# Optimization experiments

Measured on AMD Instinct MI355X. Metric: run time of the kernel, lower is better.

## Reference

```python
import jax, jax.numpy as jnp
import numpy as np

N_EMBD = 768
N_HEAD = 12
N_LAYERS = 12
VOCAB = 50257
HEAD_DIM = N_EMBD // N_HEAD
D_FF = 4 * N_EMBD
B, S = 2, 1024


def setup_inputs() -> dict:
    key = jax.random.key(0)
    ks = jax.random.split(key, 8)
    w = lambda k, shape: jax.random.normal(k, shape, jnp.float32) * 0.02
    return {
        "x": jax.random.normal(ks[0], (B, S, N_EMBD), jnp.float32),
        "Wqkv": w(ks[1], (N_LAYERS, N_EMBD, 3 * N_EMBD)),
        "bqkv": jnp.zeros((N_LAYERS, 3 * N_EMBD), jnp.float32),
        "Wo": w(ks[2], (N_LAYERS, N_EMBD, N_EMBD)),
        "bo": jnp.zeros((N_LAYERS, N_EMBD), jnp.float32),
        "W1": w(ks[3], (N_LAYERS, N_EMBD, D_FF)),
        "b1": jnp.zeros((N_LAYERS, D_FF), jnp.float32),
        "W2": w(ks[4], (N_LAYERS, D_FF, N_EMBD)),
        "b2": jnp.zeros((N_LAYERS, N_EMBD), jnp.float32),
        "ln1_g": jnp.ones((N_LAYERS, N_EMBD), jnp.float32),
        "ln1_b": jnp.zeros((N_LAYERS, N_EMBD), jnp.float32),
        "ln2_g": jnp.ones((N_LAYERS, N_EMBD), jnp.float32),
        "ln2_b": jnp.zeros((N_LAYERS, N_EMBD), jnp.float32),
        "lnf_g": jnp.ones((N_EMBD,), jnp.float32),
        "lnf_b": jnp.zeros((N_EMBD,), jnp.float32),
        "Wlm": w(ks[5], (VOCAB, N_EMBD)),
    }


def layer_norm(x, g, b, eps=1e-5):
    m = jnp.mean(x, axis=-1, keepdims=True)
    v = jnp.var(x, axis=-1, keepdims=True)
    return (x - m) * jax.lax.rsqrt(v + eps) * g + b


def reference(x, Wqkv, bqkv, Wo, bo, W1, b1, W2, b2,
              ln1_g, ln1_b, ln2_g, ln2_b, lnf_g, lnf_b, Wlm):
    b_, s_, d_ = x.shape
    # additive causal mask: (1 - tril) * -1e10
    mask = (1.0 - jnp.tril(jnp.ones((s_, s_), jnp.float32))) * -1e10
    scale = 1.0 / np.sqrt(HEAD_DIM).astype(np.float32)

    def block(h, p):
        wqkv, bq, wo, bo_, w1, b1_, w2, b2_, g1, be1, g2, be2 = p
        a = layer_norm(h, g1, be1)
        qkv = a @ wqkv + bq                      # [B,S,3D]
        q, k, v = jnp.split(qkv, 3, axis=-1)
        split = lambda t: t.reshape(b_, s_, N_HEAD, HEAD_DIM).transpose(0, 2, 1, 3)
        q, k, v = split(q), split(k), split(v)   # [B,H,S,hd]
        scores = jnp.einsum('bhqd,bhkd->bhqk', q, k) * scale + mask
        probs = jax.nn.softmax(scores, axis=-1)
        o = jnp.einsum('bhqk,bhkd->bhqd', probs, v)
        o = o.transpose(0, 2, 1, 3).reshape(b_, s_, d_)
        h = h + (o @ wo + bo_)                   # residual 1
        m = layer_norm(h, g2, be2)
        m = jax.nn.gelu(m @ w1 + b1_, approximate=False)  # torch nn.GELU (erf)
        h = h + (m @ w2 + b2_)                   # residual 2
        return h, None

    h, _ = jax.lax.scan(
        block, x,
        (Wqkv, bqkv, Wo, bo, W1, b1, W2, b2, ln1_g, ln1_b, ln2_g, ln2_b))
    h = layer_norm(h, lnf_g, lnf_b)
    return h @ Wlm.T                             # [B,S,VOCAB]
```

## Files before the change

kernel.cpp:

```cpp
#include <hip/hip_runtime.h>
#include <math.h>

typedef unsigned short u16;
typedef u16 u16x8 __attribute__((ext_vector_type(8)));
typedef u16 u16x4 __attribute__((ext_vector_type(4)));
typedef short short8 __attribute__((ext_vector_type(8)));
typedef float f32x4 __attribute__((ext_vector_type(4)));

#define NE 768
#define NH 12
#define NL 12
#define NV 50257
#define NVP 50432
#define HD 64
#define DFF 3072
#define NB 2
#define SL 1024
#define TT 2048
#define QKVD 2304

static __device__ __forceinline__ u16 f2bf(float f){
  unsigned int x; __builtin_memcpy(&x, &f, 4);
  x = (x + 0x7FFFu + ((x >> 16) & 1u)) >> 16;
  return (u16)x;
}

typedef const __attribute__((address_space(1))) unsigned int* gas1_t;
typedef __attribute__((address_space(3))) unsigned int* las3_t;
static __device__ __forceinline__ void gload16(const u16* g, u16* l){
  __builtin_amdgcn_global_load_lds((gas1_t)(const void*)g, (las3_t)(void*)l, 16, 0, 0);
}
static __device__ __forceinline__ void waitvm(int n){
  switch (n){
    case 0: asm volatile("s_waitcnt vmcnt(0)" ::: "memory"); break;
    case 3: asm volatile("s_waitcnt vmcnt(3)" ::: "memory"); break;
    case 4: asm volatile("s_waitcnt vmcnt(4)" ::: "memory"); break;
    case 6: asm volatile("s_waitcnt vmcnt(6)" ::: "memory"); break;
    default: asm volatile("s_waitcnt vmcnt(8)" ::: "memory"); break;
  }
}

__global__ void k_cvt4(const float4* __restrict__ in, u16x4* __restrict__ out, long n4){
  long i = (long)blockIdx.x * blockDim.x + threadIdx.x;
  long st = (long)gridDim.x * blockDim.x;
  for (; i < n4; i += st){
    float4 v = in[i];
    u16x4 o = { f2bf(v.x), f2bf(v.y), f2bf(v.z), f2bf(v.w) };
    out[i] = o;
  }
}

__global__ __launch_bounds__(256) void k_transpose_cvt_all(const float* __restrict__ in0,
    u16* __restrict__ out0, int K, int N){
  __shared__ u16 tile[32][33];
  const float* in = in0 + (long)blockIdx.z * K * N;
  u16* out = out0 + (long)blockIdx.z * N * K;
  int n0 = blockIdx.x * 32, k0 = blockIdx.y * 32;
#pragma unroll
  for (int i = 0; i < 4; ++i){
    int e = threadIdx.x + i * 256;
    int r = e >> 5, c = e & 31;
    tile[r][c] = f2bf(in[(long)(k0 + r) * N + (n0 + c)]);
  }
  __syncthreads();
#pragma unroll
  for (int i = 0; i < 4; ++i){
    int e = threadIdx.x + i * 256;
    int r = e >> 5, c = e & 31;
    out[(long)(n0 + r) * K + (k0 + c)] = tile[c][r];
  }
}

__global__ __launch_bounds__(256) void k_layernorm(const float* __restrict__ x,
    const float* __restrict__ g, const float* __restrict__ b, u16* __restrict__ out){
  int row = blockIdx.x;
  const float* xr = x + (long)row * NE;
  int t = threadIdx.x;
  float v[3];
  v[0] = xr[t]; v[1] = xr[t + 256]; v[2] = xr[t + 512];
  float s = v[0] + v[1] + v[2];
  float sq = v[0]*v[0] + v[1]*v[1] + v[2]*v[2];
  __shared__ float red[8];
#pragma unroll
  for (int o = 32; o; o >>= 1){ s += __shfl_xor(s, o); sq += __shfl_xor(sq, o); }
  int wid = t >> 6, lane = t & 63;
  if (!lane){ red[wid] = s; red[4 + wid] = sq; }
  __syncthreads();
  s  = red[0] + red[1] + red[2] + red[3];
  sq = red[4] + red[5] + red[6] + red[7];
  float mean = s * (1.f / NE);
  float var  = sq * (1.f / NE) - mean * mean;
  float rs = rsqrtf(var + 1e-5f);
  u16* orow = out + (long)row * NE;
#pragma unroll
  for (int i = 0; i < 3; ++i){
    int c = t + i * 256;
    orow[c] = f2bf((v[i] - mean) * rs * g[c] + b[c]);
  }
}

__global__ __launch_bounds__(256) void k_combine_ln(float* __restrict__ h,
    const float* __restrict__ part, const float* __restrict__ bias, int nsplit,
    const float* __restrict__ g, const float* __restrict__ b, u16* __restrict__ aout){
  int row = blockIdx.x;
  int t = threadIdx.x;
  float* hr = h + (long)row * NE;
  float v[3];
#pragma unroll
  for (int i = 0; i < 3; ++i){
    int c = t + i * 256;
    float acc = hr[c] + bias[c];
    for (int s = 0; s < nsplit; ++s)
      acc += part[(long)s * TT * NE + (long)row * NE + c];
    v[i] = acc;
    hr[c] = acc;
  }
  float s = v[0] + v[1] + v[2];
  float sq = v[0]*v[0] + v[1]*v[1] + v[2]*v[2];
  __shared__ float red[8];
#pragma unroll
  for (int o = 32; o; o >>= 1){ s += __shfl_xor(s, o); sq += __shfl_xor(sq, o); }
  int wid = t >> 6, lane = t & 63;
  if (!lane){ red[wid] = s; red[4 + wid] = sq; }
  __syncthreads();
  s  = red[0] + red[1] + red[2] + red[3];
  sq = red[4] + red[5] + red[6] + red[7];
  float mean = s * (1.f / NE);
  float var  = sq * (1.f / NE) - mean * mean;
  float rs = rsqrtf(var + 1e-5f);
  u16* orow = aout + (long)row * NE;
#pragma unroll
  for (int i = 0; i < 3; ++i){
    int c = t + i * 256;
    orow[c] = f2bf((v[i] - mean) * rs * g[c] + b[c]);
  }
}

__global__ __launch_bounds__(256) void k_flash(const u16* __restrict__ qkv,
    const u16* __restrict__ vt, u16* __restrict__ out){
  __shared__ u16 Ps[4][16][72];
  const int z = blockIdx.x;
  const int qt = gridDim.y - 1 - blockIdx.y;
  const int b = z / NH, h = z % NH;
  const int q0 = qt * 64;
  const int t = threadIdx.x, lane = t & 63, wid = t >> 6;
  const int lr = lane & 15, lk = lane >> 4;
  const int qr0 = q0 + wid * 16;
  const u16* Qp = qkv + (long)(b * SL + qr0 + lr) * QKVD + h * HD;
  short8 aq[2];
  aq[0] = *(const short8*)(Qp + lk * 8);
  aq[1] = *(const short8*)(Qp + 32 + lk * 8);
  const u16* Kb  = qkv + (long)(b * SL) * QKVD + NE + h * HD;
  const u16* Vtb = vt + (long)z * HD * SL;
  f32x4 o[4] = {};
  float m[4], l[4];
#pragma unroll
  for (int r = 0; r < 4; ++r){ m[r] = -3e38f; l[r] = 0.f; }
  const int nt = qt + 1;
  for (int kt = 0; kt < nt; ++kt){
    const int kv0 = kt * 64;
    short8 kb[4][2];
#pragma unroll
    for (int j = 0; j < 4; ++j)
#pragma unroll
      for (int c = 0; c < 2; ++c)
        kb[j][c] = *(const short8*)(Kb + (long)(kv0 + j * 16 + lr) * QKVD + c * 32 + lk * 8);
    f32x4 s[4] = {};
#pragma unroll
    for (int c = 0; c < 2; ++c)
#pragma unroll
      for (int j = 0; j < 4; ++j)
        s[j] = __builtin_amdgcn_mfma_f32_16x16x32_bf16(aq[c], kb[j][c], s[j], 0, 0, 0);
    const bool dm = (kt == nt - 1);
#pragma unroll
    for (int r = 0; r < 4; ++r){
      const int row = qr0 + lk * 4 + r;
      float pm = -3e38f;
#pragma unroll
      for (int j = 0; j < 4; ++j){
        float v = s[j][r] * 0.125f;
        if (dm && (kv0 + j * 16 + lr > row)) v = -3e38f;
        s[j][r] = v;
        pm = fmaxf(pm, v);
      }
#pragma unroll
      for (int off = 1; off < 16; off <<= 1) pm = fmaxf(pm, __shfl_xor(pm, off));
      float mn = fmaxf(m[r], pm);
      float f = __expf(m[r] - mn);
      m[r] = mn;
      float ps = 0.f;
#pragma unroll
      for (int j = 0; j < 4; ++j){
        float pv = __expf(s[j][r] - mn);
        ps += pv;
        Ps[wid][lk * 4 + r][j * 16 + lr] = f2bf(pv);
      }
#pragma unroll
      for (int off = 1; off < 16; off <<= 1) ps += __shfl_xor(ps, off);
      l[r] = l[r] * f + ps;
#pragma unroll
      for (int j = 0; j < 4; ++j) o[j][r] *= f;
    }
#pragma unroll
    for (int c = 0; c < 2; ++c){
      short8 pa = *(const short8*)&Ps[wid][lr][c * 32 + lk * 8];
#pragma unroll
      for (int j = 0; j < 4; ++j){
        short8 vb = *(const short8*)(Vtb + (long)(j * 16 + lr) * SL + kv0 + c * 32 + lk * 8);
        o[j] = __builtin_amdgcn_mfma_f32_16x16x32_bf16(pa, vb, o[j], 0, 0, 0);
      }
    }
  }
  u16* O = out + (long)(b * SL) * NE + h * HD;
#pragma unroll
  for (int r = 0; r < 4; ++r){
    float inv = 1.f / l[r];
    const int row = qr0 + lk * 4 + r;
#pragma unroll
    for (int j = 0; j < 4; ++j)
      O[(long)row * NE + j * 16 + lr] = f2bf(o[j][r] * inv);
  }
}

struct GemmP {
  const u16* A; const u16* B; void* C;
  const float* bias; u16* vt;
  int M, N, K, lda, ldb, ldc, mode;
  long zA, zB, zC;
};

__global__ __launch_bounds__(256) void k_gemm_bt(GemmP p){
  __shared__ u16 As[3][64 * 32];
  __shared__ u16 Bs[3][128 * 32];
  const int nwg = gridDim.x * gridDim.y;
  const int orig = blockIdx.x + blockIdx.y * gridDim.x;
  const int wg = (orig & 7) * (nwg >> 3) + (orig >> 3);
  const int m0 = (wg % gridDim.x) * 64, n0 = (wg / gridDim.x) * 128;
  const u16* A = p.A + (long)blockIdx.z * p.zA;
  const u16* B = p.B + (long)blockIdx.z * p.zB;
  const long offC = (long)blockIdx.z * p.zC;
  const int t = threadIdx.x, lane = t & 63, wid = t >> 6;
  const int wm = (wid >> 1) * 32, wn = (wid & 1) * 64;
  const int lr = lane & 15, lk = lane >> 4;
  const int srow = t >> 2;
  const int sseg = (t & 3) * 8;
  const u16* Abase  = A + (long)(m0 + srow) * p.lda + sseg;
  const u16* Bbase  = B + (long)(n0 + srow) * p.ldb + sseg;
  const u16* Bbase2 = B + (long)(n0 + 64 + srow) * p.ldb + sseg;
  auto stage = [&](int buf, int kt){
    gload16(Abase  + kt * 32, &As[buf][t * 8]);
    gload16(Bbase  + kt * 32, &Bs[buf][t * 8]);
    gload16(Bbase2 + kt * 32, &Bs[buf][(t + 256) * 8]);
  };
  f32x4 acc[2][4] = {};
  const int nk = p.K >> 5;
  stage(0, 0);
  stage(1, 1);
  int cur = 0;
  for (int kt = 0; kt < nk; ++kt){
    if (kt + 2 < nk){
      int nxt = cur + 2; if (nxt >= 3) nxt -= 3;
      stage(nxt, kt + 2);
    }
    int rem = nk - 1 - kt;
    waitvm(rem >= 2 ? 6 : rem == 1 ? 3 : 0);
    __builtin_amdgcn_s_barrier();
    short8 af[2], bfr[4];
#pragma unroll
    for (int i = 0; i < 2; ++i) af[i]  = *(const short8*)&As[cur][(wm + i * 16 + lr) * 32 + lk * 8];
#pragma unroll
    for (int j = 0; j < 4; ++j) bfr[j] = *(const short8*)&Bs[cur][(wn + j * 16 + lr) * 32 + lk * 8];
#pragma unroll
    for (int i = 0; i < 2; ++i)
#pragma unroll
      for (int j = 0; j < 4; ++j)
        acc[i][j] = __builtin_amdgcn_mfma_f32_16x16x32_bf16(af[i], bfr[j], acc[i][j], 0, 0, 0);
    asm volatile("s_waitcnt lgkmcnt(0)" ::: "memory");
    __builtin_amdgcn_s_barrier();
    cur = (cur == 2) ? 0 : cur + 1;
  }
#pragma unroll
  for (int i = 0; i < 2; ++i){
#pragma unroll
    for (int r = 0; r < 4; ++r){
      int row = m0 + wm + i * 16 + lk * 4 + r;
      if (row >= p.M) continue;
#pragma unroll
      for (int j = 0; j < 4; ++j){
        int col = n0 + wn + j * 16 + lr;
        if (col >= p.N) continue;
        float v = acc[i][j][r];
        long idx = offC + (long)row * p.ldc + col;
        if (p.mode == 5){
          v += p.bias[col];
          if (col >= 2 * NE){
            int d = col - 2 * NE;
            long vidx = (((long)(row >> 10) * NH + (d >> 6)) * HD + (d & 63)) * SL + (row & 1023);
            p.vt[vidx] = f2bf(v);
          } else {
            ((u16*)p.C)[idx] = f2bf(v);
          }
        } else if (p.mode == 2){
          v += p.bias[col];
          v = 0.5f * v * (1.f + erff(v * 0.70710678118f));
          ((u16*)p.C)[idx] = f2bf(v);
        } else {
          ((float*)p.C)[idx] = v;
        }
      }
    }
  }
}

static inline void gemm(hipStream_t s, const u16* A, int lda, const u16* B, int ldb,
    void* C, int ldc, int M, int N, int K, const float* bias, u16* vt, int mode,
    int gz = 1, long zA = 0, long zB = 0, long zC = 0){
  GemmP p{ A, B, C, bias, vt, M, N, K, lda, ldb, ldc, mode, zA, zB, zC };
  dim3 g(M / 64, (N + 127) / 128, gz);
  k_gemm_bt<<<g, 256, 0, s>>>(p);
}

__global__ __launch_bounds__(1024, 4) void k_gemm256(const u16* __restrict__ A,
    const u16* __restrict__ B, float* __restrict__ C){
  __shared__ u16 As[2][256 * 64];
  __shared__ u16 Bs[2][256 * 64];
  const int gx = gridDim.x, nwg = gx * gridDim.y;
  const int orig = blockIdx.x + blockIdx.y * gx;
  const int wg = (orig & 7) * (nwg >> 3) + (orig >> 3);
  const int m0 = (wg % gx) * 256, n0 = (wg / gx) * 256;
  const int t = threadIdx.x, lane = t & 63;
  const int lr = lane & 15, lk = lane >> 4;
  const int wid = t >> 6, wr = wid >> 2, wc = wid & 3;
  const u16* gA[2]; const u16* gB[2]; int ldst[2];
#pragma unroll
  for (int i = 0; i < 2; ++i){
    int tt = t + i * 1024, r = tt >> 3, pp = tt & 7, sl = pp ^ (r & 7);
    gA[i] = A + (long)(m0 + r) * NE + sl * 8;
    gB[i] = B + (long)(n0 + r) * NE + sl * 8;
    ldst[i] = tt * 8;
  }
  auto stage = [&](int buf, int kt){
#pragma unroll
    for (int i = 0; i < 2; ++i) gload16(gA[i] + kt * 64, &As[buf][ldst[i]]);
#pragma unroll
    for (int i = 0; i < 2; ++i) gload16(gB[i] + kt * 64, &Bs[buf][ldst[i]]);
  };
  f32x4 acc[4][4] = {};
  const int nk = NE / 64;
  stage(0, 0);
  for (int kt = 0; kt < nk; ++kt){
    const int buf = kt & 1;
    if (kt + 1 < nk){ stage(buf ^ 1, kt + 1); waitvm(4); }
    else            { waitvm(0); }
    __builtin_amdgcn_sched_barrier(0);
    __builtin_amdgcn_s_barrier();
    __builtin_amdgcn_sched_barrier(0);
    short8 bf[4][2];
#pragma unroll
    for (int nj = 0; nj < 4; ++nj)
#pragma unroll
      for (int kc = 0; kc < 2; ++kc){
        int r = wc * 64 + nj * 16 + lr;
        bf[nj][kc] = *(const short8*)&Bs[buf][r * 64 + ((kc * 32 + lk * 8) ^ ((r & 7) << 3))];
      }
#pragma unroll
    for (int mh = 0; mh < 2; ++mh){
      short8 af[2][2];
#pragma unroll
      for (int mi = 0; mi < 2; ++mi)
#pragma unroll
        for (int kc = 0; kc < 2; ++kc){
          int r = wr * 64 + (mh * 2 + mi) * 16 + lr;
          af[mi][kc] = *(const short8*)&As[buf][r * 64 + ((kc * 32 + lk * 8) ^ ((r & 7) << 3))];
        }
      __builtin_amdgcn_s_setprio(1);
#pragma unroll
      for (int mi = 0; mi < 2; ++mi)
#pragma unroll
        for (int nj = 0; nj < 4; ++nj)
#pragma unroll
          for (int kc = 0; kc < 2; ++kc)
            acc[mh * 2 + mi][nj] = __builtin_amdgcn_mfma_f32_16x16x32_bf16(af[mi][kc], bf[nj][kc], acc[mh * 2 + mi][nj], 0, 0, 0);
      __builtin_amdgcn_s_setprio(0);
    }
    asm volatile("s_waitcnt lgkmcnt(0)" ::: "memory");
    __builtin_amdgcn_sched_barrier(0);
    __builtin_amdgcn_s_barrier();
  }
#pragma unroll
  for (int mi = 0; mi < 4; ++mi)
#pragma unroll
    for (int r = 0; r < 4; ++r){
      int row = m0 + wr * 64 + mi * 16 + lk * 4 + r;
#pragma unroll
      for (int nj = 0; nj < 4; ++nj){
        int col = n0 + wc * 64 + nj * 16 + lr;
        if (col < NV) C[(long)row * NV + col] = acc[mi][nj][r];
      }
    }
}

extern "C" void kernel_launch(void* const* d_in, const int* in_sizes, int n_in,
                              void* d_out, int out_size, void* d_ws, size_t ws_size,
                              hipStream_t stream){
  (void)in_sizes; (void)n_in; (void)out_size; (void)ws_size;
  const float* x    = (const float*)d_in[0];
  const float* Wqkv = (const float*)d_in[1];
  const float* bqkv = (const float*)d_in[2];
  const float* Wo   = (const float*)d_in[3];
  const float* bo   = (const float*)d_in[4];
  const float* W1   = (const float*)d_in[5];
  const float* b1   = (const float*)d_in[6];
  const float* W2   = (const float*)d_in[7];
  const float* b2   = (const float*)d_in[8];
  const float* ln1g = (const float*)d_in[9];
  const float* ln1b = (const float*)d_in[10];
  const float* ln2g = (const float*)d_in[11];
  const float* ln2b = (const float*)d_in[12];
  const float* lnfg = (const float*)d_in[13];
  const float* lnfb = (const float*)d_in[14];
  const float* Wlm  = (const float*)d_in[15];

  char* ws = (char*)d_ws;
  size_t off = 0;
  auto alloc = [&](size_t bytes){ void* p = ws + off; off += (bytes + 255) & ~255UL; return p; };
  float* h      = (float*)alloc((size_t)TT * NE * 4);
  u16*   a      = (u16*)  alloc((size_t)TT * NE * 2);
  u16*   qkv    = (u16*)  alloc((size_t)TT * QKVD * 2);
  u16*   vtbuf  = (u16*)  alloc((size_t)NB * NH * HD * SL * 2);
  u16*   attno  = (u16*)  alloc((size_t)TT * NE * 2);
  u16*   ffm    = (u16*)  alloc((size_t)TT * DFF * 2);
  float* part   = (float*)alloc((size_t)4 * TT * NE * 4);
  u16*   wqkvT  = (u16*)  alloc((size_t)NL * QKVD * NE * 2);
  u16*   woT    = (u16*)  alloc((size_t)NL * NE * NE * 2);
  u16*   w1T    = (u16*)  alloc((size_t)NL * DFF * NE * 2);
  u16*   w2T    = (u16*)  alloc((size_t)NL * NE * DFF * 2);
  u16*   wlmB   = (u16*)  alloc((size_t)NVP * NE * 2);

  hipMemcpyAsync(h, x, (size_t)TT * NE * 4, hipMemcpyDeviceToDevice, stream);
  k_transpose_cvt_all<<<dim3(QKVD / 32, NE / 32, NL), 256, 0, stream>>>(Wqkv, wqkvT, NE, QKVD);
  k_transpose_cvt_all<<<dim3(NE / 32, NE / 32, NL),   256, 0, stream>>>(Wo,   woT,   NE, NE);
  k_transpose_cvt_all<<<dim3(DFF / 32, NE / 32, NL),  256, 0, stream>>>(W1,   w1T,   NE, DFF);
  k_transpose_cvt_all<<<dim3(NE / 32, DFF / 32, NL),  256, 0, stream>>>(W2,   w2T,   DFF, NE);
  k_cvt4<<<2048, 256, 0, stream>>>((const float4*)Wlm, (u16x4*)wlmB, (long)NV * NE / 4);
  hipMemsetAsync(wlmB + (size_t)NV * NE, 0, (size_t)(NVP - NV) * NE * 2, stream);

  k_layernorm<<<TT, 256, 0, stream>>>(h, ln1g, ln1b, a);

  for (int L = 0; L < NL; ++L){
    gemm(stream, a, NE, wqkvT + (size_t)L * QKVD * NE, NE, qkv, QKVD, TT, QKVD, NE,
         bqkv + (size_t)L * QKVD, vtbuf, 5);
    k_flash<<<dim3(NB * NH, SL / 64), 256, 0, stream>>>(qkv, vtbuf, attno);
    gemm(stream, attno, NE, woT + (size_t)L * NE * NE, NE, part, NE, TT, NE, 384,
         nullptr, nullptr, 3, 2, 384, 384, (long)TT * NE);
    k_combine_ln<<<TT, 256, 0, stream>>>(h, part, bo + (size_t)L * NE, 2,
         ln2g + (size_t)L * NE, ln2b + (size_t)L * NE, a);
    gemm(stream, a, NE, w1T + (size_t)L * DFF * NE, NE, ffm, DFF, TT, DFF, NE,
         b1 + (size_t)L * DFF, nullptr, 2);
    gemm(stream, ffm, DFF, w2T + (size_t)L * NE * DFF, DFF, part, NE, TT, NE, 768,
         nullptr, nullptr, 3, 4, 768, 768, (long)TT * NE);
    const float* gn = (L + 1 < NL) ? ln1g + (size_t)(L + 1) * NE : lnfg;
    const float* bn = (L + 1 < NL) ? ln1b + (size_t)(L + 1) * NE : lnfb;
    k_combine_ln<<<TT, 256, 0, stream>>>(h, part, b2 + (size_t)L * NE, 4, gn, bn, a);
  }
  k_gemm256<<<dim3(TT / 256, NVP / 256), 1024, 0, stream>>>(a, wlmB, (float*)d_out);
}
```

Baseline: 2.509 ms.

## Halve flash query tile and retile LM-head GEMM with triple-buffered K=32 stages

The flash-attention kernel now uses 32-row query tiles with two waves per block instead of 64 rows with four. This doubles the grid and cuts wasted causal work in the last KV tile. The LM-head GEMM moves from 1024 threads with a K=64 double buffer to 512 threads, each wave covering 128x64 outputs, with a K=32 triple-buffered pipeline and a 4-way swizzle. This trades more accumulator registers per thread and lower occupancy for deeper prefetch and more MFMA work per LDS fragment.

Result: no change. 2.474 ms (-1.4%).

```diff
diff --git a/kernel.cpp b/kernel.cpp
--- a/kernel.cpp
+++ b/kernel.cpp
@@ -136,16 +136,15 @@
   }
 }
 
-__global__ __launch_bounds__(256) void k_flash(const u16* __restrict__ qkv,
+__global__ __launch_bounds__(128) void k_flash(const u16* __restrict__ qkv,
     const u16* __restrict__ vt, u16* __restrict__ out){
-  __shared__ u16 Ps[4][16][72];
+  __shared__ u16 Ps[2][16][72];
   const int z = blockIdx.x;
   const int qt = gridDim.y - 1 - blockIdx.y;
   const int b = z / NH, h = z % NH;
-  const int q0 = qt * 64;
   const int t = threadIdx.x, lane = t & 63, wid = t >> 6;
   const int lr = lane & 15, lk = lane >> 4;
-  const int qr0 = q0 + wid * 16;
+  const int qr0 = qt * 32 + wid * 16;
   const u16* Qp = qkv + (long)(b * SL + qr0 + lr) * QKVD + h * HD;
   short8 aq[2];
   aq[0] = *(const short8*)(Qp + lk * 8);
@@ -156,7 +155,7 @@
   float m[4], l[4];
 #pragma unroll
   for (int r = 0; r < 4; ++r){ m[r] = -3e38f; l[r] = 0.f; }
-  const int nt = qt + 1;
+  const int nt = (qt * 32 + 31) / 64 + 1;
   for (int kt = 0; kt < nt; ++kt){
     const int kv0 = kt * 64;
     short8 kb[4][2];
@@ -320,10 +319,10 @@
   k_gemm_bt<<<g, 256, 0, s>>>(p);
 }
 
-__global__ __launch_bounds__(1024, 4) void k_gemm256(const u16* __restrict__ A,
+__global__ __launch_bounds__(512, 1) void k_gemm256(const u16* __restrict__ A,
     const u16* __restrict__ B, float* __restrict__ C){
-  __shared__ u16 As[2][256 * 64];
-  __shared__ u16 Bs[2][256 * 64];
+  __shared__ u16 As[3][256 * 32];
+  __shared__ u16 Bs[3][256 * 32];
   const int gx = gridDim.x, nwg = gx * gridDim.y;
   const int orig = blockIdx.x + blockIdx.y * gx;
   const int wg = (orig & 7) * (nwg >> 3) + (orig >> 3);
@@ -334,64 +333,78 @@
   const u16* gA[2]; const u16* gB[2]; int ldst[2];
 #pragma unroll
   for (int i = 0; i < 2; ++i){
-    int tt = t + i * 1024, r = tt >> 3, pp = tt & 7, sl = pp ^ (r & 7);
+    int idx = t + i * 512, r = idx >> 2, pp = idx & 3, sl = pp ^ (r & 3);
     gA[i] = A + (long)(m0 + r) * NE + sl * 8;
     gB[i] = B + (long)(n0 + r) * NE + sl * 8;
-    ldst[i] = tt * 8;
+    ldst[i] = idx * 8;
   }
   auto stage = [&](int buf, int kt){
 #pragma unroll
-    for (int i = 0; i < 2; ++i) gload16(gA[i] + kt * 64, &As[buf][ldst[i]]);
-#pragma unroll
-    for (int i = 0; i < 2; ++i) gload16(gB[i] + kt * 64, &Bs[buf][ldst[i]]);
+    for (int i = 0; i < 2; ++i) gload16(gA[i] + kt * 32, &As[buf][ldst[i]]);
+#pragma unroll
+    for (int i = 0; i < 2; ++i) gload16(gB[i] + kt * 32, &Bs[buf][ldst[i]]);
   };
-  f32x4 acc[4][4] = {};
-  const int nk = NE / 64;
+  f32x4 acc[8][4] = {};
+  const int nk = NE / 32;
   stage(0, 0);
+  stage(1, 1);
+  int cur = 0;
   for (int kt = 0; kt < nk; ++kt){
-    const int buf = kt & 1;
-    if (kt + 1 < nk){ stage(buf ^ 1, kt + 1); waitvm(4); }
-    else            { waitvm(0); }
+    if (kt + 2 < nk){
+      int nxt = cur + 2; if (nxt >= 3) nxt -= 3;
+      stage(nxt, kt + 2);
+    }
+    int rem = nk - 1 - kt;
+    waitvm(rem >= 2 ? 8 : rem == 1 ? 4 : 0);
     __builtin_amdgcn_sched_barrier(0);
     __builtin_amdgcn_s_barrier();
     __builtin_amdgcn_sched_barrier(0);
-    short8 bf[4][2];
-#pragma unroll
-    for (int nj = 0; nj < 4; ++nj)
-#pragma unroll
-      for (int kc = 0; kc < 2; ++kc){
-        int r = wc * 64 + nj * 16 + lr;
-        bf[nj][kc] = *(const short8*)&Bs[buf][r * 64 + ((kc * 32 + lk * 8) ^ ((r & 7) << 3))];
-      }
-#pragma unroll
-    for (int mh = 0; mh < 2; ++mh){
-      short8 af[2][2];
-#pragma unroll
-      for (int mi = 0; mi < 2; ++mi)
-#pragma unroll
-        for (int kc = 0; kc < 2; ++kc){
-          int r = wr * 64 + (mh * 2 + mi) * 16 + lr;
-          af[mi][kc] = *(const short8*)&As[buf][r * 64 + ((kc * 32 + lk * 8) ^ ((r & 7) << 3))];
-        }
+    short8 bf[4];
+#pragma unroll
+    for (int nj = 0; nj < 4; ++nj){
+      int r = wc * 64 + nj * 16 + lr;
+      bf[nj] = *(const short8*)&Bs[cur][r * 32 + ((lk ^ (r & 3)) * 8)];
+    }
+    {
+      short8 af[4];
+#pragma unroll
+      for (int mi = 0; mi < 4; ++mi){
+        int r = wr * 128 + mi * 16 + lr;
+        af[mi] = *(const short8*)&As[cur][r * 32 + ((lk ^ (r & 3)) * 8)];
+      }
       __builtin_amdgcn_s_setprio(1);
 #pragma unroll
-      for (int mi = 0; mi < 2; ++mi)
+      for (int mi = 0; mi < 4; ++mi)
 #pragma unroll
         for (int nj = 0; nj < 4; ++nj)
-#pragma unroll
-          for (int kc = 0; kc < 2; ++kc)
-            acc[mh * 2 + mi][nj] = __builtin_amdgcn_mfma_f32_16x16x32_bf16(af[mi][kc], bf[nj][kc], acc[mh * 2 + mi][nj], 0, 0, 0);
+          acc[mi][nj] = __builtin_amdgcn_mfma_f32_16x16x32_bf16(af[mi], bf[nj], acc[mi][nj], 0, 0, 0);
+      __builtin_amdgcn_s_setprio(0);
+    }
+    {
+      short8 af[4];
+#pragma unroll
+      for (int mi = 0; mi < 4; ++mi){
+        int r = wr * 128 + (mi + 4) * 16 + lr;
+        af[mi] = *(const short8*)&As[cur][r * 32 + ((lk ^ (r & 3)) * 8)];
+      }
+      __builtin_amdgcn_s_setprio(1);
+#pragma unroll
+      for (int mi = 0; mi < 4; ++mi)
+#pragma unroll
+        for (int nj = 0; nj < 4; ++nj)
+          acc[mi + 4][nj] = __builtin_amdgcn_mfma_f32_16x16x32_bf16(af[mi], bf[nj], acc[mi + 4][nj], 0, 0, 0);
       __builtin_amdgcn_s_setprio(0);
     }
     asm volatile("s_waitcnt lgkmcnt(0)" ::: "memory");
     __builtin_amdgcn_sched_barrier(0);
     __builtin_amdgcn_s_barrier();
-  }
-#pragma unroll
-  for (int mi = 0; mi < 4; ++mi)
+    cur = (cur == 2) ? 0 : cur + 1;
+  }
+#pragma unroll
+  for (int mi = 0; mi < 8; ++mi)
 #pragma unroll
     for (int r = 0; r < 4; ++r){
-      int row = m0 + wr * 64 + mi * 16 + lk * 4 + r;
+      int row = m0 + wr * 128 + mi * 16 + lk * 4 + r;
 #pragma unroll
       for (int nj = 0; nj < 4; ++nj){
         int col = n0 + wc * 64 + nj * 16 + lr;
@@ -450,7 +463,7 @@
   for (int L = 0; L < NL; ++L){
     gemm(stream, a, NE, wqkvT + (size_t)L * QKVD * NE, NE, qkv, QKVD, TT, QKVD, NE,
          bqkv + (size_t)L * QKVD, vtbuf, 5);
-    k_flash<<<dim3(NB * NH, SL / 64), 256, 0, stream>>>(qkv, vtbuf, attno);
+    k_flash<<<dim3(NB * NH, SL / 32), 128, 0, stream>>>(qkv, vtbuf, attno);
     gemm(stream, attno, NE, woT + (size_t)L * NE * NE, NE, part, NE, TT, NE, 384,
          nullptr, nullptr, 3, 2, 384, 384, (long)TT * NE);
     k_combine_ln<<<TT, 256, 0, stream>>>(h, part, bo + (size_t)L * NE, 2,
@@ -463,5 +476,5 @@
     const float* bn = (L + 1 < NL) ? ln1b + (size_t)(L + 1) * NE : lnfb;
     k_combine_ln<<<TT, 256, 0, stream>>>(h, part, b2 + (size_t)L * NE, 4, gn, bn, a);
   }
-  k_gemm256<<<dim3(TT / 256, NVP / 256), 1024, 0, stream>>>(a, wlmB, (float*)d_out);
-}
+  k_gemm256<<<dim3(TT / 256, NVP / 256), 512, 0, stream>>>(a, wlmB, (float*)d_out);
+}
```
